# Optimization experiments

Hardware: AMD Instinct MI355X
Metric: run time of the kernel (lower is better)

The kernel has to match this reference:

```python
import jax, jax.numpy as jnp
import numpy as np

HIDDEN_DIM = 1024
NUM_HEADS = 16
HEAD_DIM = HIDDEN_DIM // NUM_HEADS


def setup_inputs() -> dict:
    key = jax.random.key(0)
    ks = jax.random.split(key, 9)
    s = 1.0 / np.sqrt(HIDDEN_DIM)
    x = jax.random.normal(ks[0], (2, 2048, HIDDEN_DIM), dtype=jnp.float32)
    Wq = jax.random.uniform(ks[1], (HIDDEN_DIM, HIDDEN_DIM), jnp.float32, -s, s)
    bq = jax.random.uniform(ks[2], (HIDDEN_DIM,), jnp.float32, -s, s)
    Wk = jax.random.uniform(ks[3], (HIDDEN_DIM, HIDDEN_DIM), jnp.float32, -s, s)
    bk = jax.random.uniform(ks[4], (HIDDEN_DIM,), jnp.float32, -s, s)
    Wv = jax.random.uniform(ks[5], (HIDDEN_DIM, HIDDEN_DIM), jnp.float32, -s, s)
    bv = jax.random.uniform(ks[6], (HIDDEN_DIM,), jnp.float32, -s, s)
    Wo = jax.random.uniform(ks[7], (HIDDEN_DIM, HIDDEN_DIM), jnp.float32, -s, s)
    bo = jax.random.uniform(ks[8], (HIDDEN_DIM,), jnp.float32, -s, s)
    return {"x": x, "Wq": Wq, "bq": bq, "Wk": Wk, "bk": bk,
            "Wv": Wv, "bv": bv, "Wo": Wo, "bo": bo}


def reference(x, Wq, bq, Wk, bk, Wv, bv, Wo, bo):
    B, M, D = x.shape
    H, Dh = NUM_HEADS, HEAD_DIM
    # projections -> [B, H, M, Dh]
    def split_heads(t):
        return t.reshape(B, M, H, Dh).transpose(0, 2, 1, 3)
    q = split_heads(x @ Wq.T + bq)
    k = split_heads(x @ Wk.T + bk)
    v = split_heads(x @ Wv.T + bv)
    scores = jnp.einsum('bhmd,bhnd->bhmn', q, k) / np.sqrt(Dh).astype(np.float32)
    # multiplicative diagonal-zero mask: zero the diagonal of the score matrix
    diag_zero = 1.0 - jnp.eye(M, dtype=scores.dtype)  # [M, M]
    scores = scores * diag_zero
    attn = jax.nn.softmax(scores, axis=-1)
    context = jnp.einsum('bhmn,bhnd->bhmd', attn, v)
    context = context.transpose(0, 2, 1, 3).reshape(B, M, D)
    return context @ Wo.T + bo
```

## Files before the change

kernel.cpp:

```cpp
#include <hip/hip_runtime.h>
#include <stdint.h>

typedef _Float16 f16;
typedef __attribute__((ext_vector_type(8))) _Float16 f16x8;
typedef __attribute__((ext_vector_type(4))) _Float16 f16x4;
typedef __attribute__((ext_vector_type(2))) __fp16 fp16x2;
typedef __attribute__((ext_vector_type(4))) float f32x4;

#define HD 1024
#define NH 16
#define DH 64
#define BB 2
#define MM 2048
#define BH (BB*NH)
#define MT (BB*MM)

__device__ __forceinline__ void gl_lds16(const f16* g, f16* l) {
    __builtin_amdgcn_global_load_lds((const __attribute__((address_space(1))) uint32_t*)g,
                                     (__attribute__((address_space(3))) uint32_t*)l, 16, 0, 0);
}

__device__ __forceinline__ float fexp2(float x) {
    float r; asm("v_exp_f32 %0, %1" : "=v"(r) : "v"(x)); return r;
}

__global__ void cvt_all(const float* __restrict__ x,  const float* __restrict__ wq,
                        const float* __restrict__ wk, const float* __restrict__ wv,
                        const float* __restrict__ wo, f16* __restrict__ dst) {
    const int XN4 = MT * HD / 4;
    const int WN4 = HD * HD / 4;
    int i = blockIdx.x * blockDim.x + threadIdx.x;
    if (i >= XN4 + 4 * WN4) return;
    const float* s; int off;
    if (i < XN4) { s = x; off = i; }
    else {
        int k = i - XN4, wsel = k >> 18;
        off = k & (WN4 - 1);
        s = wsel == 0 ? wq : wsel == 1 ? wk : wsel == 2 ? wv : wo;
    }
    float4 v = ((const float4*)s)[off];
    f16x4 h;
    h[0] = (f16)v.x; h[1] = (f16)v.y; h[2] = (f16)v.z; h[3] = (f16)v.w;
    ((f16x4*)dst)[i] = h;
}

template<int MODE>
__global__ __launch_bounds__(256, 3) void gemm_m97(const f16* __restrict__ A,
                                                   const f16* __restrict__ W,
                                                   const float* __restrict__ b0,
                                                   const float* __restrict__ b1,
                                                   const float* __restrict__ b2,
                                                   f16* __restrict__ oh,
                                                   float* __restrict__ of) {
    __shared__ f16 As[128 * 32];
    __shared__ f16 Bs[128 * 32];
    const int bid = blockIdx.x;
    int bn, bm;
    if (MODE == 0) { int xcd = bid & 7, r = bid >> 3; bn = xcd * 3 + (r >> 5); bm = r & 31; }
    else           { bn = bid & 7; bm = bid >> 3; }
    const int t = threadIdx.x, w = t >> 6, lane = t & 63;
    const int wr = w >> 1, wc = w & 1, lr = lane & 15, lg = lane >> 4;
    f32x4 acc[4][4] = {};

    const int srow = w * 16 + (lane >> 2);
    const int schunk = lane & 3;
    const f16* Ab = A + (size_t)(bm * 128) * HD;
    const f16* Wb = W + (size_t)(bn * 128) * HD;
    f16* Asw = As + w * 512;
    f16* Bsw = Bs + w * 512;

    #pragma unroll
    for (int i = 0; i < 2; i++) {
        int r = i * 64 + srow;
        int gc = ((schunk ^ ((r >> 1) & 3)) * 8);
        gl_lds16(Ab + (size_t)r * HD + gc, Asw + i * 2048);
        gl_lds16(Wb + (size_t)r * HD + gc, Bsw + i * 2048);
    }

    for (int k0 = 0;;) {
        __syncthreads();
        f16x8 af[4], bf[4];
        #pragma unroll
        for (int i = 0; i < 4; i++) {
            int ra = wr * 64 + i * 16 + lr;
            af[i] = *(const f16x8*)(As + ra * 32 + ((lg ^ ((ra >> 1) & 3)) * 8));
            int rb = wc * 64 + i * 16 + lr;
            bf[i] = *(const f16x8*)(Bs + rb * 32 + ((lg ^ ((rb >> 1) & 3)) * 8));
        }
        #pragma unroll
        for (int i = 0; i < 4; i++)
            #pragma unroll
            for (int j = 0; j < 4; j++)
                acc[i][j] = __builtin_amdgcn_mfma_f32_16x16x32_f16(af[i], bf[j], acc[i][j], 0, 0, 0);
        k0 += 32;
        if (k0 >= HD) break;
        __syncthreads();
        #pragma unroll
        for (int i = 0; i < 2; i++) {
            int r = i * 64 + srow;
            int gc = ((schunk ^ ((r >> 1) & 3)) * 8);
            gl_lds16(Ab + (size_t)r * HD + k0 + gc, Asw + i * 2048);
            gl_lds16(Wb + (size_t)r * HD + k0 + gc, Bsw + i * 2048);
        }
    }

    if (MODE == 0) {
        const int mat = bn >> 3;
        const float* bp = mat == 0 ? b0 : mat == 1 ? b1 : b2;
        f16* base = oh + (size_t)mat * BH * MM * DH;
        #pragma unroll
        for (int i = 0; i < 4; i++) {
            #pragma unroll
            for (int j = 0; j < 4; j++) {
                int n = bn * 128 + wc * 64 + j * 16 + lr;
                int nn = n & 1023, h = nn >> 6, dh = nn & 63;
                float bvv = bp[nn];
                int mg0 = bm * 128 + wr * 64 + i * 16 + lg * 4;
                int b = mg0 >> 11, mmr0 = mg0 & 2047;
                if (mat == 2) {
                    f16x4 o;
                    #pragma unroll
                    for (int r = 0; r < 4; r++) o[r] = (f16)(acc[i][j][r] + bvv);
                    *(f16x4*)(base + ((size_t)((b * NH + h) * DH + dh)) * MM + mmr0) = o;
                } else {
                    float sc = (mat == 0) ? 0.1803368801111204f : 1.0f;
                    #pragma unroll
                    for (int r = 0; r < 4; r++)
                        base[((size_t)((b * NH + h) * MM + mmr0 + r)) * DH + dh] =
                            (f16)((acc[i][j][r] + bvv) * sc);
                }
            }
        }
    } else {
        #pragma unroll
        for (int i = 0; i < 4; i++)
            #pragma unroll
            for (int j = 0; j < 4; j++) {
                int n = bn * 128 + wc * 64 + j * 16 + lr;
                float bvv = b0[n];
                #pragma unroll
                for (int r = 0; r < 4; r++) {
                    int mg = bm * 128 + wr * 64 + i * 16 + lg * 4 + r;
                    of[(size_t)mg * HD + n] = acc[i][j][r] + bvv;
                }
            }
    }
}

__global__ __launch_bounds__(256, 4) void attn_kernel(const f16* __restrict__ Q,
                                                      const f16* __restrict__ K,
                                                      const f16* __restrict__ Vt,
                                                      f16* __restrict__ ctx) {
    __shared__ f16 Kl[2][64][64];
    __shared__ f16 Vl[2][64][64];
    __shared__ f16 Pl[4][16][64];
    const int bid = blockIdx.x;
    const int xcd = bid & 7, idx = bid >> 3;
    const int bh = xcd * 4 + (idx >> 5);
    const int qblk = idx & 31;

    const int t = threadIdx.x, w = t >> 6, lane = t & 63;
    const int lr = lane & 15, lg = lane >> 4;
    const int q0 = qblk * 64 + w * 16;

    const f16* Qb = Q + (size_t)bh * MM * DH;
    const f16* Kb = K + (size_t)bh * MM * DH;
    const f16* Vb = Vt + (size_t)bh * DH * MM;

    const int srow = lane >> 3;
    const int sxc = ((lane & 7) ^ srow) * 8;
    const int lds_r = w * 16;

    f16x8 qfr[2];
    #pragma unroll
    for (int c = 0; c < 2; c++)
        qfr[c] = *(const f16x8*)(Qb + (size_t)(q0 + lr) * DH + c * 32 + lg * 8);

    f32x4 po[4] = {};
    float lsum = 0.f;
    const int sw = (lr & 7) * 8;
    f16* Pw = &Pl[w][0][0];
    const int ko0 = (lg * 8) ^ sw, ko1 = (32 + lg * 8) ^ sw;

    #pragma unroll
    for (int i = 0; i < 2; i++) {
        int row = lds_r + i * 8 + srow;
        gl_lds16(Kb + (size_t)row * DH + sxc, &Kl[0][lds_r + i * 8][0]);
        gl_lds16(Vb + (size_t)row * MM + sxc, &Vl[0][lds_r + i * 8][0]);
    }
    __syncthreads();

#define ATTN_BODY(CUR, IT)                                                                   \
    {                                                                                        \
        const int it_ = (IT);                                                                \
        if (it_ < 31) {                                                                      \
            const int jn = (it_ + 1) * 64;                                                   \
            _Pragma("unroll")                                                                \
            for (int i = 0; i < 2; i++) {                                                    \
                int row = lds_r + i * 8 + srow;                                              \
                gl_lds16(Kb + (size_t)(jn + row) * DH + sxc, &Kl[CUR ^ 1][lds_r + i * 8][0]);\
                gl_lds16(Vb + (size_t)row * MM + jn + sxc, &Vl[CUR ^ 1][lds_r + i * 8][0]); \
            }                                                                                \
        }                                                                                    \
        f32x4 sa[4] = {};                                                                    \
        __builtin_amdgcn_s_setprio(1);                                                       \
        _Pragma("unroll")                                                                    \
        for (int f = 0; f < 4; f++) {                                                        \
            const f16* kr = &Kl[CUR][f * 16 + lr][0];                                        \
            f16x8 k0 = *(const f16x8*)(kr + ko0);                                            \
            f16x8 k1 = *(const f16x8*)(kr + ko1);                                            \
            sa[f] = __builtin_amdgcn_mfma_f32_16x16x32_f16(k0, qfr[0], sa[f], 0, 0, 0);      \
            sa[f] = __builtin_amdgcn_mfma_f32_16x16x32_f16(k1, qfr[1], sa[f], 0, 0, 0);      \
        }                                                                                    \
        __builtin_amdgcn_s_setprio(0);                                                       \
        if (it_ == qblk) {                   \
            int q = q0 + lr;                                                                 \
            _Pragma("unroll")                                                                \
            for (int f = 0; f < 4; f++)                                                      \
                _Pragma("unroll")                                                            \
                for (int r = 0; r < 4; r++)                                                  \
                    if (q == it_ * 64 + f * 16 + lg * 4 + r) sa[f][r] = 0.f;                 \
        }                                                                                    \
        _Pragma("unroll")                                                                    \
        for (int f = 0; f < 4; f++) {                                                        \
            float p0 = fexp2(sa[f][0]), p1 = fexp2(sa[f][1]);                                \
            float p2 = fexp2(sa[f][2]), p3 = fexp2(sa[f][3]);                                \
            lsum += (p0 + p1) + (p2 + p3);                                                   \
            fp16x2 lo = __builtin_amdgcn_cvt_pkrtz(p0, p1);                                  \
            fp16x2 hi = __builtin_amdgcn_cvt_pkrtz(p2, p3);                                  \
            uint2 pr; pr.x = __builtin_bit_cast(uint32_t, lo);                               \
            pr.y = __builtin_bit_cast(uint32_t, hi);                                         \
            *(f16x4*)(Pw + lr * 64 + ((f * 16 + lg * 4) ^ sw)) =                             \
                __builtin_bit_cast(f16x4, pr);                                               \
        }                                                                                    \
        asm volatile("s_waitcnt lgkmcnt(0)" ::: "memory");      \
        f16x8 pf0 = *(const f16x8*)(Pw + lr * 64 + ko0);                                     \
        f16x8 pf1 = *(const f16x8*)(Pw + lr * 64 + ko1);                                     \
        __builtin_amdgcn_s_setprio(1);                                                       \
        _Pragma("unroll")                                                                    \
        for (int df = 0; df < 4; df++) {                                                     \
            const f16* vr = &Vl[CUR][df * 16 + lr][0];                                       \
            f16x8 v0 = *(const f16x8*)(vr + ko0);                                            \
            f16x8 v1 = *(const f16x8*)(vr + ko1);                                            \
            po[df] = __builtin_amdgcn_mfma_f32_16x16x32_f16(v0, pf0, po[df], 0, 0, 0);       \
            po[df] = __builtin_amdgcn_mfma_f32_16x16x32_f16(v1, pf1, po[df], 0, 0, 0);       \
        }                                                                                    \
        __builtin_amdgcn_s_setprio(0);                                                       \
        __syncthreads();                   \
    }

    for (int itp = 0; itp < 16; ++itp) {
        ATTN_BODY(0, 2 * itp)
        ATTN_BODY(1, 2 * itp + 1)
    }
#undef ATTN_BODY

    lsum += __shfl_xor(lsum, 16);
    lsum += __shfl_xor(lsum, 32);
    const int b = bh >> 4, h = bh & 15;
    const float inv = 1.f / lsum;
    f16* cp = ctx + ((size_t)(b * MM + q0 + lr)) * HD + h * DH;
    #pragma unroll
    for (int df = 0; df < 4; df++) {
        f16x4 o;
        #pragma unroll
        for (int r = 0; r < 4; r++) o[r] = (f16)(po[df][r] * inv);
        *(f16x4*)(cp + df * 16 + lg * 4) = o;
    }
}

extern "C" void kernel_launch(void* const* d_in, const int* in_sizes, int n_in,
                              void* d_out, int out_size, void* d_ws, size_t ws_size,
                              hipStream_t stream) {
    const float* x  = (const float*)d_in[0];
    const float* Wq = (const float*)d_in[1];
    const float* bq = (const float*)d_in[2];
    const float* Wk = (const float*)d_in[3];
    const float* bk = (const float*)d_in[4];
    const float* Wv = (const float*)d_in[5];
    const float* bv = (const float*)d_in[6];
    const float* Wo = (const float*)d_in[7];
    const float* bo = (const float*)d_in[8];
    float* out = (float*)d_out;

    f16* xh  = (f16*)d_ws;
    f16* wqh = xh  + (size_t)MT * HD;
    f16* woh = wqh + (size_t)3 * HD * HD;
    f16* Qh  = woh + (size_t)HD * HD;
    f16* ctxh= Qh  + (size_t)3 * BH * MM * DH;

    const int total4 = MT * HD / 4 + HD * HD;
    cvt_all<<<(total4 + 255) / 256, 256, 0, stream>>>(x, Wq, Wk, Wv, Wo, xh);

    gemm_m97<0><<<768, 256, 0, stream>>>(xh, wqh, bq, bk, bv, Qh, nullptr);

    attn_kernel<<<1024, 256, 0, stream>>>(Qh, Qh + (size_t)BH * MM * DH,
                                          Qh + (size_t)2 * BH * MM * DH, ctxh);

    gemm_m97<1><<<256, 256, 0, stream>>>(ctxh, woh, bo, nullptr, nullptr, nullptr, out);
}
```

Measured before the change: 120.2 us.

## Double-buffer GEMM LDS tiles and replace full syncs with partial vmcnt waits

The GEMM now keeps two LDS buffers for the A and W tiles and issues the next k-slice's global-to-LDS loads before computing on the current one. It waits with s_waitcnt vmcnt(4) so only the older loads must land before the barrier. The attention loop likewise swaps __syncthreads for an explicit vmcnt wait plus s_barrier, letting the prefetch of the next K/V tile stay in flight. The GEMM's LDS use doubles, which may lower occupancy under launch_bounds(256,3), and correctness now depends on the hand-counted vmcnt values.

```diff
diff --git a/kernel.cpp b/kernel.cpp
--- a/kernel.cpp
+++ b/kernel.cpp
@@ -52,8 +52,8 @@
                                                    const float* __restrict__ b2,
                                                    f16* __restrict__ oh,
                                                    float* __restrict__ of) {
-    __shared__ f16 As[128 * 32];
-    __shared__ f16 Bs[128 * 32];
+    __shared__ f16 As[2][128 * 32];
+    __shared__ f16 Bs[2][128 * 32];
     const int bid = blockIdx.x;
     int bn, bm;
     if (MODE == 0) { int xcd = bid & 7, r = bid >> 3; bn = xcd * 3 + (r >> 5); bm = r & 31; }
@@ -66,43 +66,49 @@
     const int schunk = lane & 3;
     const f16* Ab = A + (size_t)(bm * 128) * HD;
     const f16* Wb = W + (size_t)(bn * 128) * HD;
-    f16* Asw = As + w * 512;
-    f16* Bsw = Bs + w * 512;
-
-    #pragma unroll
-    for (int i = 0; i < 2; i++) {
-        int r = i * 64 + srow;
-        int gc = ((schunk ^ ((r >> 1) & 3)) * 8);
-        gl_lds16(Ab + (size_t)r * HD + gc, Asw + i * 2048);
-        gl_lds16(Wb + (size_t)r * HD + gc, Bsw + i * 2048);
-    }
-
-    for (int k0 = 0;;) {
-        __syncthreads();
-        f16x8 af[4], bf[4];
-        #pragma unroll
-        for (int i = 0; i < 4; i++) {
-            int ra = wr * 64 + i * 16 + lr;
-            af[i] = *(const f16x8*)(As + ra * 32 + ((lg ^ ((ra >> 1) & 3)) * 8));
-            int rb = wc * 64 + i * 16 + lr;
-            bf[i] = *(const f16x8*)(Bs + rb * 32 + ((lg ^ ((rb >> 1) & 3)) * 8));
-        }
-        #pragma unroll
-        for (int i = 0; i < 4; i++)
-            #pragma unroll
-            for (int j = 0; j < 4; j++)
-                acc[i][j] = __builtin_amdgcn_mfma_f32_16x16x32_f16(af[i], bf[j], acc[i][j], 0, 0, 0);
-        k0 += 32;
-        if (k0 >= HD) break;
-        __syncthreads();
-        #pragma unroll
-        for (int i = 0; i < 2; i++) {
-            int r = i * 64 + srow;
-            int gc = ((schunk ^ ((r >> 1) & 3)) * 8);
-            gl_lds16(Ab + (size_t)r * HD + k0 + gc, Asw + i * 2048);
-            gl_lds16(Wb + (size_t)r * HD + k0 + gc, Bsw + i * 2048);
-        }
-    }
+
+#define GSTAGE(BUF, K0)                                                         \
+    _Pragma("unroll")                                                           \
+    for (int i = 0; i < 2; i++) {                                               \
+        int r = i * 64 + srow;                                                  \
+        int gc = ((schunk ^ ((r >> 1) & 3)) * 8);                               \
+        gl_lds16(Ab + (size_t)r * HD + (K0) + gc, &As[BUF][w * 512 + i * 2048]);\
+        gl_lds16(Wb + (size_t)r * HD + (K0) + gc, &Bs[BUF][w * 512 + i * 2048]);\
+    }
+
+#define GCOMP(BUF)                                                              \
+    {                                                                           \
+        f16x8 af[4], bf[4];                                                     \
+        _Pragma("unroll")                                                       \
+        for (int i = 0; i < 4; i++) {                                           \
+            int ra = wr * 64 + i * 16 + lr;                                     \
+            af[i] = *(const f16x8*)(&As[BUF][ra * 32 + ((lg ^ ((ra >> 1) & 3)) * 8)]); \
+            int rb = wc * 64 + i * 16 + lr;                                     \
+            bf[i] = *(const f16x8*)(&Bs[BUF][rb * 32 + ((lg ^ ((rb >> 1) & 3)) * 8)]); \
+        }                                                                       \
+        _Pragma("unroll")                                                       \
+        for (int i = 0; i < 4; i++)                                             \
+            _Pragma("unroll")                                                   \
+            for (int j = 0; j < 4; j++)                                         \
+                acc[i][j] = __builtin_amdgcn_mfma_f32_16x16x32_f16(af[i], bf[j], acc[i][j], 0, 0, 0); \
+    }
+
+    GSTAGE(0, 0)
+    int cur = 0;
+    for (int k0 = 0; k0 < HD - 32; k0 += 32) {
+        GSTAGE(cur ^ 1, k0 + 32)
+        asm volatile("s_waitcnt vmcnt(4)" ::: "memory");
+        __builtin_amdgcn_s_barrier();
+        GCOMP(cur)
+        asm volatile("" ::: "memory");
+        __builtin_amdgcn_s_barrier();
+        cur ^= 1;
+    }
+    asm volatile("s_waitcnt vmcnt(0)" ::: "memory");
+    __builtin_amdgcn_s_barrier();
+    GCOMP(cur)
+#undef GSTAGE
+#undef GCOMP
 
     if (MODE == 0) {
         const int mat = bn >> 3;
@@ -188,9 +194,8 @@
         gl_lds16(Kb + (size_t)row * DH + sxc, &Kl[0][lds_r + i * 8][0]);
         gl_lds16(Vb + (size_t)row * MM + sxc, &Vl[0][lds_r + i * 8][0]);
     }
-    __syncthreads();
-
-#define ATTN_BODY(CUR, IT)                                                                   \
+
+#define ATTN_BODY(CUR, IT, VMN)                                                              \
     {                                                                                        \
         const int it_ = (IT);                                                                \
         if (it_ < 31) {                                                                      \
@@ -202,6 +207,8 @@
                 gl_lds16(Vb + (size_t)row * MM + jn + sxc, &Vl[CUR ^ 1][lds_r + i * 8][0]); \
             }                                                                                \
         }                                                                                    \
+        asm volatile("s_waitcnt vmcnt(" #VMN ")" ::: "memory");   \
+        __builtin_amdgcn_s_barrier();                                \
         f32x4 sa[4] = {};                                                                    \
         __builtin_amdgcn_s_setprio(1);                                                       \
         _Pragma("unroll")                                                                    \
@@ -246,13 +253,16 @@
             po[df] = __builtin_amdgcn_mfma_f32_16x16x32_f16(v1, pf1, po[df], 0, 0, 0);       \
         }                                                                                    \
         __builtin_amdgcn_s_setprio(0);                                                       \
-        __syncthreads();                   \
-    }
-
-    for (int itp = 0; itp < 16; ++itp) {
-        ATTN_BODY(0, 2 * itp)
-        ATTN_BODY(1, 2 * itp + 1)
-    }
+        asm volatile("" ::: "memory");                                                       \
+        __builtin_amdgcn_s_barrier();          \
+    }
+
+    for (int itp = 0; itp < 15; ++itp) {
+        ATTN_BODY(0, 2 * itp, 4)
+        ATTN_BODY(1, 2 * itp + 1, 4)
+    }
+    ATTN_BODY(0, 30, 4)
+    ATTN_BODY(1, 31, 0)
 #undef ATTN_BODY
 
     lsum += __shfl_xor(lsum, 16);
```

After: 122.5 us. No clear change (+1.9%).

## Split attention waves 2x2 over queries and KV columns with LDS reduction

Applied to the files above, without the earlier changes.

Each wave now handles 32 query rows against half of each 64-key tile, rather than 16 query rows against the whole tile. This reuses K and V fragments across two query fragments and halves V LDS reads per MFMA. Partial outputs and row sums from the two KV-half waves are combined through LDS at the end. The full __syncthreads is replaced by a vmcnt wait plus a raw barrier, and launch bounds drop to 3 waves per EU to allow more registers, which costs occupancy.

```diff
diff --git a/kernel.cpp b/kernel.cpp
--- a/kernel.cpp
+++ b/kernel.cpp
@@ -147,13 +147,13 @@
     }
 }
 
-__global__ __launch_bounds__(256, 4) void attn_kernel(const f16* __restrict__ Q,
+__global__ __launch_bounds__(256, 3) void attn_kernel(const f16* __restrict__ Q,
                                                       const f16* __restrict__ K,
                                                       const f16* __restrict__ Vt,
                                                       f16* __restrict__ ctx) {
     __shared__ f16 Kl[2][64][64];
     __shared__ f16 Vl[2][64][64];
-    __shared__ f16 Pl[4][16][64];
+    __shared__ f16 Pl[4][32][40];
     const int bid = blockIdx.x;
     const int xcd = bid & 7, idx = bid >> 3;
     const int bh = xcd * 4 + (idx >> 5);
@@ -161,7 +161,9 @@
 
     const int t = threadIdx.x, w = t >> 6, lane = t & 63;
     const int lr = lane & 15, lg = lane >> 4;
-    const int q0 = qblk * 64 + w * 16;
+    const int wq = w >> 1, wkv = w & 1;
+    const int q0B = qblk * 64 + wq * 32;
+    const int kvb = wkv * 32;
 
     const f16* Qb = Q + (size_t)bh * MM * DH;
     const f16* Kb = K + (size_t)bh * MM * DH;
@@ -171,16 +173,19 @@
     const int sxc = ((lane & 7) ^ srow) * 8;
     const int lds_r = w * 16;
 
-    f16x8 qfr[2];
+    f16x8 qfr[2][2];
     #pragma unroll
-    for (int c = 0; c < 2; c++)
-        qfr[c] = *(const f16x8*)(Qb + (size_t)(q0 + lr) * DH + c * 32 + lg * 8);
-
-    f32x4 po[4] = {};
-    float lsum = 0.f;
+    for (int qf = 0; qf < 2; qf++)
+        #pragma unroll
+        for (int c = 0; c < 2; c++)
+            qfr[qf][c] = *(const f16x8*)(Qb + (size_t)(q0B + qf * 16 + lr) * DH + c * 32 + lg * 8);
+
+    f32x4 po[4][2] = {};
+    float lsum0 = 0.f, lsum1 = 0.f;
     const int sw = (lr & 7) * 8;
+    const int ko0 = (lg * 8) ^ sw, ko1 = (32 + lg * 8) ^ sw;
+    const int vko = (kvb + lg * 8) ^ sw;
     f16* Pw = &Pl[w][0][0];
-    const int ko0 = (lg * 8) ^ sw, ko1 = (32 + lg * 8) ^ sw;
 
     #pragma unroll
     for (int i = 0; i < 2; i++) {
@@ -188,9 +193,8 @@
         gl_lds16(Kb + (size_t)row * DH + sxc, &Kl[0][lds_r + i * 8][0]);
         gl_lds16(Vb + (size_t)row * MM + sxc, &Vl[0][lds_r + i * 8][0]);
     }
-    __syncthreads();
-
-#define ATTN_BODY(CUR, IT)                                                                   \
+
+#define ATTN_BODY(CUR, IT, VMN)                                                              \
     {                                                                                        \
         const int it_ = (IT);                                                                \
         if (it_ < 31) {                                                                      \
@@ -202,70 +206,109 @@
                 gl_lds16(Vb + (size_t)row * MM + jn + sxc, &Vl[CUR ^ 1][lds_r + i * 8][0]); \
             }                                                                                \
         }                                                                                    \
-        f32x4 sa[4] = {};                                                                    \
+        asm volatile("s_waitcnt vmcnt(" #VMN ")" ::: "memory");                              \
+        __builtin_amdgcn_s_barrier();                                                        \
+                        \
+        f32x4 s00 = {}, s01 = {}, s10 = {}, s11 = {};                         \
         __builtin_amdgcn_s_setprio(1);                                                       \
+        {                                                                                    \
+            const f16* kr0 = &Kl[CUR][kvb + lr][0];                                          \
+            f16x8 ka = *(const f16x8*)(kr0 + ko0);                                           \
+            f16x8 kb = *(const f16x8*)(kr0 + ko1);                                           \
+            s00 = __builtin_amdgcn_mfma_f32_16x16x32_f16(ka, qfr[0][0], s00, 0, 0, 0);       \
+            s00 = __builtin_amdgcn_mfma_f32_16x16x32_f16(kb, qfr[0][1], s00, 0, 0, 0);       \
+            s01 = __builtin_amdgcn_mfma_f32_16x16x32_f16(ka, qfr[1][0], s01, 0, 0, 0);       \
+            s01 = __builtin_amdgcn_mfma_f32_16x16x32_f16(kb, qfr[1][1], s01, 0, 0, 0);       \
+            const f16* kr1 = &Kl[CUR][kvb + 16 + lr][0];                                     \
+            f16x8 kc = *(const f16x8*)(kr1 + ko0);                                           \
+            f16x8 kd = *(const f16x8*)(kr1 + ko1);                                           \
+            s10 = __builtin_amdgcn_mfma_f32_16x16x32_f16(kc, qfr[0][0], s10, 0, 0, 0);       \
+            s10 = __builtin_amdgcn_mfma_f32_16x16x32_f16(kd, qfr[0][1], s10, 0, 0, 0);       \
+            s11 = __builtin_amdgcn_mfma_f32_16x16x32_f16(kc, qfr[1][0], s11, 0, 0, 0);       \
+            s11 = __builtin_amdgcn_mfma_f32_16x16x32_f16(kd, qfr[1][1], s11, 0, 0, 0);       \
+        }                                                                                    \
+        __builtin_amdgcn_s_setprio(0);                                                       \
+                \
+        if (it_ == qblk && wq == wkv) {                                                      \
+            int rr = lr - lg * 4;                                                            \
+            if (rr >= 0 && rr < 4) { s00[rr] = 0.f; s11[rr] = 0.f; }                         \
+        }                                                                                    \
+                         \
         _Pragma("unroll")                                                                    \
-        for (int f = 0; f < 4; f++) {                                                        \
-            const f16* kr = &Kl[CUR][f * 16 + lr][0];                                        \
-            f16x8 k0 = *(const f16x8*)(kr + ko0);                                            \
-            f16x8 k1 = *(const f16x8*)(kr + ko1);                                            \
-            sa[f] = __builtin_amdgcn_mfma_f32_16x16x32_f16(k0, qfr[0], sa[f], 0, 0, 0);      \
-            sa[f] = __builtin_amdgcn_mfma_f32_16x16x32_f16(k1, qfr[1], sa[f], 0, 0, 0);      \
-        }                                                                                    \
-        __builtin_amdgcn_s_setprio(0);                                                       \
-        if (it_ == qblk) {                   \
-            int q = q0 + lr;                                                                 \
-            _Pragma("unroll")                                                                \
-            for (int f = 0; f < 4; f++)                                                      \
-                _Pragma("unroll")                                                            \
-                for (int r = 0; r < 4; r++)                                                  \
-                    if (q == it_ * 64 + f * 16 + lg * 4 + r) sa[f][r] = 0.f;                 \
-        }                                                                                    \
-        _Pragma("unroll")                                                                    \
-        for (int f = 0; f < 4; f++) {                                                        \
-            float p0 = fexp2(sa[f][0]), p1 = fexp2(sa[f][1]);                                \
-            float p2 = fexp2(sa[f][2]), p3 = fexp2(sa[f][3]);                                \
-            lsum += (p0 + p1) + (p2 + p3);                                                   \
+        for (int u = 0; u < 4; u++) {                                                        \
+            const f32x4 sv = (u == 0) ? s00 : (u == 1) ? s01 : (u == 2) ? s10 : s11;         \
+            const int fq = u >> 1, qf = u & 1;                                               \
+            float p0 = fexp2(sv[0]), p1 = fexp2(sv[1]);                                      \
+            float p2 = fexp2(sv[2]), p3 = fexp2(sv[3]);                                      \
+            if (qf == 0) lsum0 += (p0 + p1) + (p2 + p3);                                     \
+            else         lsum1 += (p0 + p1) + (p2 + p3);                                     \
             fp16x2 lo = __builtin_amdgcn_cvt_pkrtz(p0, p1);                                  \
             fp16x2 hi = __builtin_amdgcn_cvt_pkrtz(p2, p3);                                  \
             uint2 pr; pr.x = __builtin_bit_cast(uint32_t, lo);                               \
             pr.y = __builtin_bit_cast(uint32_t, hi);                                         \
-            *(f16x4*)(Pw + lr * 64 + ((f * 16 + lg * 4) ^ sw)) =                             \
+            *(f16x4*)(Pw + (qf * 16 + lr) * 40 + fq * 16 + lg * 4) =                         \
                 __builtin_bit_cast(f16x4, pr);                                               \
         }                                                                                    \
         asm volatile("s_waitcnt lgkmcnt(0)" ::: "memory");      \
-        f16x8 pf0 = *(const f16x8*)(Pw + lr * 64 + ko0);                                     \
-        f16x8 pf1 = *(const f16x8*)(Pw + lr * 64 + ko1);                                     \
+        f16x8 pf0 = *(const f16x8*)(Pw + lr * 40 + lg * 8);                                  \
+        f16x8 pf1 = *(const f16x8*)(Pw + (16 + lr) * 40 + lg * 8);                           \
+                                             \
         __builtin_amdgcn_s_setprio(1);                                                       \
         _Pragma("unroll")                                                                    \
         for (int df = 0; df < 4; df++) {                                                     \
             const f16* vr = &Vl[CUR][df * 16 + lr][0];                                       \
-            f16x8 v0 = *(const f16x8*)(vr + ko0);                                            \
-            f16x8 v1 = *(const f16x8*)(vr + ko1);                                            \
-            po[df] = __builtin_amdgcn_mfma_f32_16x16x32_f16(v0, pf0, po[df], 0, 0, 0);       \
-            po[df] = __builtin_amdgcn_mfma_f32_16x16x32_f16(v1, pf1, po[df], 0, 0, 0);       \
+            f16x8 va = *(const f16x8*)(vr + vko);                                            \
+            po[df][0] = __builtin_amdgcn_mfma_f32_16x16x32_f16(va, pf0, po[df][0], 0, 0, 0); \
+            po[df][1] = __builtin_amdgcn_mfma_f32_16x16x32_f16(va, pf1, po[df][1], 0, 0, 0); \
         }                                                                                    \
         __builtin_amdgcn_s_setprio(0);                                                       \
-        __syncthreads();                   \
-    }
-
-    for (int itp = 0; itp < 16; ++itp) {
-        ATTN_BODY(0, 2 * itp)
-        ATTN_BODY(1, 2 * itp + 1)
-    }
+        asm volatile("" ::: "memory");                                                       \
+        __builtin_amdgcn_s_barrier();                                                        \
+    }
+
+    for (int itp = 0; itp < 15; ++itp) {
+        ATTN_BODY(0, 2 * itp, 4)
+        ATTN_BODY(1, 2 * itp + 1, 4)
+    }
+    ATTN_BODY(0, 30, 4)
+    ATTN_BODY(1, 31, 0)
 #undef ATTN_BODY
 
-    lsum += __shfl_xor(lsum, 16);
-    lsum += __shfl_xor(lsum, 32);
-    const int b = bh >> 4, h = bh & 15;
-    const float inv = 1.f / lsum;
-    f16* cp = ctx + ((size_t)(b * MM + q0 + lr)) * HD + h * DH;
-    #pragma unroll
-    for (int df = 0; df < 4; df++) {
-        f16x4 o;
-        #pragma unroll
-        for (int r = 0; r < 4; r++) o[r] = (f16)(po[df][r] * inv);
-        *(f16x4*)(cp + df * 16 + lg * 4) = o;
+    lsum0 += __shfl_xor(lsum0, 16); lsum0 += __shfl_xor(lsum0, 32);
+    lsum1 += __shfl_xor(lsum1, 16); lsum1 += __shfl_xor(lsum1, 32);
+    __syncthreads();
+    float* shf = (float*)(&Kl[0][0][0]);
+    float* shl = (float*)(&Vl[0][0][0]);
+    const int xi = wq * 64 + lane;
+    if (wkv == 1) {
+        float* d = shf + (size_t)xi * 32;
+        #pragma unroll
+        for (int df = 0; df < 4; df++) {
+            *(f32x4*)(d + df * 8)     = po[df][0];
+            *(f32x4*)(d + df * 8 + 4) = po[df][1];
+        }
+        shl[xi * 2]     = lsum0;
+        shl[xi * 2 + 1] = lsum1;
+    }
+    __syncthreads();
+    if (wkv == 0) {
+        const float* s = shf + (size_t)xi * 32;
+        const float inv0 = 1.f / (lsum0 + shl[xi * 2]);
+        const float inv1 = 1.f / (lsum1 + shl[xi * 2 + 1]);
+        const int b = bh >> 4, hh = bh & 15;
+        #pragma unroll
+        for (int qf = 0; qf < 2; qf++) {
+            const float inv = qf ? inv1 : inv0;
+            f16* cp = ctx + ((size_t)(b * MM + q0B + qf * 16 + lr)) * HD + hh * DH;
+            #pragma unroll
+            for (int df = 0; df < 4; df++) {
+                f16x4 o;
+                #pragma unroll
+                for (int r = 0; r < 4; r++)
+                    o[r] = (f16)((po[df][qf][r] + s[df * 8 + qf * 4 + r]) * inv);
+                *(f16x4*)(cp + df * 16 + lg * 4) = o;
+            }
+        }
     }
 }
 
```

New measurement: 132.3 us. 10.0% more time.
